# Kernel tuning notes

Hardware: AMD Instinct MI355X
Metric: run time of the kernel (lower is better)

The kernel has to match this reference:

```python
import jax, jax.numpy as jnp
import numpy as np

N_HEADS = 8
EPS = 1e-8


def _build_gp_map():
    # Cl(4,1) geometric-product structure constants. Blade index = 5-bit mask,
    # e1..e5 = bits 0..4; metric (+,+,+,+,-): e5 (bit 4) squares to -1.
    def pc(n):
        return bin(n).count("1")
    g = np.zeros((32, 32, 32), np.float32)
    for a in range(32):
        for b in range(32):
            swaps = 0
            aa = a >> 1
            while aa:
                swaps += pc(aa & b)
                aa >>= 1
            sign = -1.0 if (swaps & 1) else 1.0
            if (a & b) & 0b10000:  # shared e5 factor contributes -1
                sign = -sign
            g[a, b, a ^ b] = sign
    return g

GP_MAP = jnp.asarray(_build_gp_map())          # (32,32,32)
BIVEC_IDX = jnp.array([3, 5, 6, 9, 10, 12, 17, 18, 20, 24])  # grade-2 blades
SCALAR_VECTOR_IDX = np.array([0, 1, 2, 4, 8, 16])            # grade-0 + grade-1


def normalize_cl41(x):
    return x / jnp.sqrt(jnp.sum(x * x, axis=-1, keepdims=True) + EPS)


def geometric_linear(w, x):
    # w: (O,I,32), x: (...,I,32) -> (...,O,32)
    wg = jnp.einsum('oij,jlk->oilk', w, GP_MAP)     # fold gp_map into weight
    out = jnp.einsum('oilk,...il->...ok', wg, x)
    return normalize_cl41(out)


def _init_weight(key, out_f, in_f):
    # Grade-aware Xavier: only scalar + vector lanes are nonzero.
    std = 1.0 / np.sqrt(in_f * 32)
    vals = jax.random.normal(key, (out_f, in_f, len(SCALAR_VECTOR_IDX)), jnp.float32) * std
    w = jnp.zeros((out_f, in_f, 32), jnp.float32)
    return w.at[:, :, SCALAR_VECTOR_IDX].set(vals)


def setup_inputs() -> dict:
    key = jax.random.key(0)
    kx, kq, kk, kv, ko = jax.random.split(key, 5)
    B, S, D = 2, 384, 128
    x = jax.random.normal(kx, (B, S, D, 32), jnp.float32)
    return {
        'x': x,
        'wq': _init_weight(kq, D, D),
        'wk': _init_weight(kk, D, D),
        'wv': _init_weight(kv, D, D),
        'wo': _init_weight(ko, D, D),
        'attn_lambda': jnp.float32(0.1),
    }


def reference(x, wq, wk, wv, wo, attn_lambda):
    B, S, D, _ = x.shape
    H = N_HEADS
    hd = D // H
    def split_heads(t):  # (B,S,D,32) -> (B,H,S,hd,32)
        return t.reshape(B, S, H, hd, 32).transpose(0, 2, 1, 3, 4)
    q = split_heads(geometric_linear(wq, x))
    k = split_heads(geometric_linear(wk, x))
    v = split_heads(geometric_linear(wv, x))

    # Geometric product Q*K contracted over head_dim, then over gp_map lanes.
    qg = jnp.einsum('bhsdi,ijk->bhsdjk', q, GP_MAP)      # (B,H,S,hd,32,32)
    raw_mv = jnp.einsum('bhsdjk,bhxdj->bhsxk', qg, k)    # (B,H,S,S,32)
    raw_mv = normalize_cl41(raw_mv)

    scalar_part = raw_mv[..., 0]
    biv = raw_mv[..., BIVEC_IDX]
    bivector_norm = jnp.sqrt(jnp.sum(biv * biv, axis=-1) + EPS)
    score = (scalar_part + attn_lambda * bivector_norm) / np.sqrt(hd).astype(np.float32)
    attn_probs = jax.nn.softmax(score, axis=-1)          # (B,H,S,S)

    out = jnp.einsum('bhsx,bhxdl->bhsdl', attn_probs, v)  # (B,H,S,hd,32)
    out = out.transpose(0, 2, 1, 3, 4).reshape(B, S, D, 32)
    return geometric_linear(wo, out)
```

## Files before the change

kernel.cpp:

```cpp
#include <hip/hip_runtime.h>
#include <math.h>

#define BB    2
#define SS    384
#define DD    128
#define NH    8
#define HDIM  16
#define NBH   16
#define BS    768

typedef unsigned int   u32;
typedef unsigned short u16;
typedef __attribute__((ext_vector_type(8))) short short8;
typedef __attribute__((ext_vector_type(4))) float f32x4;

struct SignTab { float v[32][32]; };
constexpr int popcnt32c(int x){ int c=0; for(int i=0;i<32;i++) c += (x>>i)&1; return c; }
constexpr int signgp_int(int a, int b){
  int swaps=0; int aa=a>>1;
  while(aa){ swaps += popcnt32c(aa & b); aa >>= 1; }
  int s = (swaps & 1) ? -1 : 1;
  if ((a & b) & 16) s = -s;
  return s;
}
constexpr SignTab make_signs(){
  SignTab t{};
  for(int a=0;a<32;a++) for(int b=0;b<32;b++)
    t.v[a][b] = (float)signgp_int(a,b);
  return t;
}
constexpr SignTab GPS = make_signs();

struct MaskTab { u32 v[4][8][4][4]; };
constexpr MaskTab mkmask(){
  MaskTab t{};
  for(int w=0;w<4;w++) for(int u=0;u<8;u++) for(int q=0;q<4;q++) for(int r=0;r<4;r++){
    u32 m = 0;
    for(int h=0;h<2;h++){
      int j = 2*r + h;
      int i = (q<<3) | j;
      int c = (w<<3) | u;
      if (signgp_int(i, i^c) < 0) m |= (h ? 0x80000000u : 0x8000u);
    }
    t.v[w][u][q][r] = m;
  }
  return t;
}
constexpr MaskTab MT = mkmask();

__device__ __forceinline__ u16 f2bf(float f){
  u32 x = __float_as_uint(f);
  return (u16)((x + 0x7FFFu + ((x>>16)&1u)) >> 16);
}
__device__ __forceinline__ float bf2f(u16 h){
  return __uint_as_float(((u32)h) << 16);
}

__global__ __launch_bounds__(256) void repack_wb(const float* __restrict__ wq,
                                                 const float* __restrict__ wk,
                                                 const float* __restrict__ wv,
                                                 const float* __restrict__ wo,
                                                 u16* __restrict__ wpk2){
  int idx = blockIdx.x*256 + threadIdx.x;
  int p = blockIdx.y;
  const float* w = (p==0)?wq:(p==1)?wk:(p==2)?wv:wo;
  int o   = idx / 768;
  int rem = idx - o*768;
  int jp  = rem >> 7;
  int i   = rem & 127;
  const int SV[6] = {0,1,2,4,8,16};
  wpk2[p*98304 + idx] = f2bf(w[(o*128 + i)*32 + SV[jp]]);
}

#define XLS 33
__global__ __launch_bounds__(256) void gather_k(const void* __restrict__ src,
                                                int src_bf16,
                                                u16* __restrict__ xg){
  __shared__ float xl[2*128*XLS];
  int t = threadIdx.x;
  int bs0 = blockIdx.x*2;
  int bsl = t >> 7, i = t & 127;

  float row[32];
  if (src_bf16){
    const uint4* s4 = (const uint4*)((const u16*)src + (((size_t)(bs0+bsl)*128 + i)*32));
    #pragma unroll
    for(int r=0;r<4;r++){
      uint4 v = s4[r];
      u32 ww[4] = {v.x,v.y,v.z,v.w};
      #pragma unroll
      for(int h=0;h<4;h++){
        row[r*8 + 2*h    ] = __uint_as_float(ww[h] << 16);
        row[r*8 + 2*h + 1] = __uint_as_float(ww[h] & 0xFFFF0000u);
      }
    }
  } else {
    const float4* s4 = (const float4*)((const float*)src + (((size_t)(bs0+bsl)*128 + i)*32));
    #pragma unroll
    for(int r=0;r<8;r++){
      float4 v = s4[r];
      row[r*4+0]=v.x; row[r*4+1]=v.y; row[r*4+2]=v.z; row[r*4+3]=v.w;
    }
  }
  float* xrow = xl + bsl*128*XLS + i*XLS;
  #pragma unroll
  for(int l=0;l<32;l++) xrow[l] = row[l];
  __syncthreads();

  const int SV[6] = {0,1,2,4,8,16};
  u32* xg32 = (u32*)xg;
  #pragma unroll 4
  for(int r=0;r<96;r++){
    int wr = t + r*256;
    int k   = wr / 768;
    int rem = wr - k*768;
    int bl  = rem / 384;
    int r2  = rem - bl*384;
    int jp  = r2 >> 6;
    int ip  = r2 & 63;
    int i2  = ip*2;
    int b   = SV[jp] ^ k;
    float sg = GPS.v[SV[jp]][b];
    const float* base = xl + bl*128*XLS;
    float f0 = base[ i2   *XLS + b] * sg;
    float f1 = base[(i2+1)*XLS + b] * sg;
    u32 pk = (u32)f2bf(f0) | ((u32)f2bf(f1) << 16);
    xg32[((size_t)k*768 + bs0 + bl)*384 + jp*64 + ip] = pk;
  }
}

#define LSTR 40
__global__ __launch_bounds__(256) void gemm_proj(const u16* __restrict__ xg,
                                                 const u16* __restrict__ wpkA,
                                                 u16* __restrict__ tmpA){
  __shared__ __align__(16) u16 As[128*LSTR];
  __shared__ __align__(16) u16 Bs[128*LSTR];
  int t = threadIdx.x;
  int Mt = blockIdx.x, k = blockIdx.y, p = blockIdx.z;
  const u16* wpk = wpkA + (size_t)p*98304;
  u16* tmp = tmpA + (size_t)p*32*768*128;

  int w = t >> 6, lane = t & 63;
  int q = lane >> 4, n16 = lane & 15;
  int wm = w >> 1, wn = w & 1;

  f32x4 acc[4][4];
  #pragma unroll
  for(int a=0;a<4;a++)
    #pragma unroll
    for(int b=0;b<4;b++) acc[a][b] = (f32x4){0.f,0.f,0.f,0.f};

  int r0 = t>>2, c0 = (t&3)*8;
  int r1 = (t+256)>>2, c1 = ((t+256)&3)*8;
  const u16* Aab = xg + ((size_t)k*768 + Mt*128)*768;

  uint4 pa0, pa1, pb0, pb1;
  {
    pa0 = *(const uint4*)(Aab + (size_t)r0*768 + c0);
    pa1 = *(const uint4*)(Aab + (size_t)r1*768 + c1);
    pb0 = *(const uint4*)(wpk + (size_t)r0*768 + c0);
    pb1 = *(const uint4*)(wpk + (size_t)r1*768 + c1);
  }

  for(int kt=0; kt<24; kt++){
    __syncthreads();
    *(uint4*)(As + r0*LSTR + c0) = pa0;
    *(uint4*)(As + r1*LSTR + c1) = pa1;
    *(uint4*)(Bs + r0*LSTR + c0) = pb0;
    *(uint4*)(Bs + r1*LSTR + c1) = pb1;
    __syncthreads();
    if (kt < 23){
      int kn = (kt+1)*32;
      pa0 = *(const uint4*)(Aab + (size_t)r0*768 + kn + c0);
      pa1 = *(const uint4*)(Aab + (size_t)r1*768 + kn + c1);
      pb0 = *(const uint4*)(wpk + (size_t)r0*768 + kn + c0);
      pb1 = *(const uint4*)(wpk + (size_t)r1*768 + kn + c1);
    }
    short8 a[4], b[4];
    #pragma unroll
    for(int mi=0;mi<4;mi++)
      a[mi] = *(const short8*)(As + (wm*64 + mi*16 + n16)*LSTR + q*8);
    #pragma unroll
    for(int ni=0;ni<4;ni++)
      b[ni] = *(const short8*)(Bs + (wn*64 + ni*16 + n16)*LSTR + q*8);
    #pragma unroll
    for(int mi=0;mi<4;mi++)
      #pragma unroll
      for(int ni=0;ni<4;ni++)
        acc[mi][ni] = __builtin_amdgcn_mfma_f32_16x16x32_bf16(a[mi], b[ni], acc[mi][ni], 0,0,0);
  }

  #pragma unroll
  for(int mi=0;mi<4;mi++){
    #pragma unroll
    for(int r=0;r<4;r++){
      int m = Mt*128 + wm*64 + mi*16 + q*4 + r;
      #pragma unroll
      for(int ni=0;ni<4;ni++){
        int n = wn*64 + ni*16 + n16;
        tmp[((size_t)k*768 + m)*128 + n] = f2bf(acc[mi][ni][r]);
      }
    }
  }
}

__global__ __launch_bounds__(256) void norm3(const u16* __restrict__ tmpA,
                                             u16* __restrict__ qhb,
                                             u16* __restrict__ khb,
                                             u16* __restrict__ vbb){
  int z = blockIdx.y;
  const u16* tmp = tmpA + (size_t)z*32*768*128;
  u16* dst = (z==0)?qhb:(z==1)?khb:vbb;
  int t = threadIdx.x;
  int bsl = t >> 7, o = t & 127;
  int bs = blockIdx.x*2 + bsl;

  float a[32];
  float ssum = 1e-8f;
  #pragma unroll
  for(int k=0;k<32;k++){
    a[k] = bf2f(tmp[((size_t)k*768 + bs)*128 + o]);
    ssum = fmaf(a[k], a[k], ssum);
  }
  float inv = 1.0f / sqrtf(ssum);

  int b = bs / SS, s = bs - b*SS;
  int h = o >> 4, d = o & 15;
  uint4* og4 = (uint4*)(dst + (((size_t)(b*NH + h)*SS + s)*512 + d*32));
  #pragma unroll
  for(int l=0;l<4;l++){
    uint4 v;
    v.x = (u32)f2bf(a[8*l+0]*inv) | ((u32)f2bf(a[8*l+1]*inv)<<16);
    v.y = (u32)f2bf(a[8*l+2]*inv) | ((u32)f2bf(a[8*l+3]*inv)<<16);
    v.z = (u32)f2bf(a[8*l+4]*inv) | ((u32)f2bf(a[8*l+5]*inv)<<16);
    v.w = (u32)f2bf(a[8*l+6]*inv) | ((u32)f2bf(a[8*l+7]*inv)<<16);
    og4[l] = v;
  }
}

__global__ __launch_bounds__(256) void norm_out(const u16* __restrict__ tmp,
                                                float* __restrict__ dst){
  int t = threadIdx.x;
  int bsl = t >> 7, o = t & 127;
  int bs = blockIdx.x*2 + bsl;

  float a[32];
  float ssum = 1e-8f;
  #pragma unroll
  for(int k=0;k<32;k++){
    a[k] = bf2f(tmp[((size_t)k*768 + bs)*128 + o]);
    ssum = fmaf(a[k], a[k], ssum);
  }
  float inv = 1.0f / sqrtf(ssum);
  float4* og = (float4*)(dst + ((size_t)bs*128 + o)*32);
  #pragma unroll
  for(int l4=0;l4<8;l4++){
    float4 v;
    v.x = a[4*l4+0]*inv; v.y = a[4*l4+1]*inv;
    v.z = a[4*l4+2]*inv; v.w = a[4*l4+3]*inv;
    og[l4] = v;
  }
}

#define TVS 528
__global__ __launch_bounds__(256) void transpose_v(const u16* __restrict__ vb,
                                                   u16* __restrict__ vt){
  __shared__ __align__(16) u16 vl[32*TVS];
  int t = threadIdx.x;
  int xt = blockIdx.x, bh = blockIdx.y;
  const u16* src = vb + ((size_t)bh*SS + xt*32)*512;
  #pragma unroll
  for(int j=0;j<8;j++){
    int f = t + j*256; int row = f>>6, c = (f&63)*8;
    *(uint4*)(vl + row*TVS + c) = *(const uint4*)(src + (size_t)row*512 + c);
  }
  __syncthreads();
  u16* dst = vt + (size_t)bh*512*SS + xt*32;
  #pragma unroll
  for(int j=0;j<8;j++){
    int f = t + j*256; int dl = f>>2, c4 = (f&3)*8;
    u16 tmp[8];
    #pragma unroll
    for(int e=0;e<8;e++) tmp[e] = vl[(c4+e)*TVS + dl];
    *(uint4*)(dst + (size_t)dl*SS + c4) = *(uint4*)tmp;
  }
}

#define QSTR 264
__global__ __launch_bounds__(256,2) void scores_mfma(const u16* __restrict__ qh,
                                                     const u16* __restrict__ kh,
                                                     float* __restrict__ sc,
                                                     const float* __restrict__ lam){
  __shared__ __align__(16) u16 smem[(64+16)*QSTR];
  u16* qs = smem;
  u16* ks = smem + 64*QSTR;
  int t = threadIdx.x;
  int xt = blockIdx.x, st = blockIdx.y, bh = blockIdx.z;
  int w = t >> 6, lane = t & 63, q = lane >> 4, mn = lane & 15;

  u32 FM[8][4];
  #pragma unroll
  for(int u=0;u<8;u++)
    #pragma unroll
    for(int r=0;r<4;r++) FM[u][r] = MT.v[w][u][q][r];

  f32x4 acc[4][8];
  #pragma unroll
  for(int mi=0;mi<4;mi++)
    #pragma unroll
    for(int u=0;u<8;u++) acc[mi][u] = (f32x4){0.f,0.f,0.f,0.f};

  for(int h=0; h<2; h++){
    __syncthreads();
    const u16* qbase = qh + ((size_t)bh*SS + st*64)*512 + h*256;
    const u16* kbase = kh + ((size_t)bh*SS + xt*16)*512 + h*256;
    #pragma unroll
    for(int j=0;j<8;j++){
      int f = t + j*256;
      int row = f>>5, c = (f&31)*8;
      *(uint4*)(qs + row*QSTR + c) = *(const uint4*)(qbase + (size_t)row*512 + c);
    }
    #pragma unroll
    for(int j=0;j<2;j++){
      int f = t + j*256;
      int row = f>>5, c = (f&31)*8;
      *(uint4*)(ks + row*QSTR + c) = *(const uint4*)(kbase + (size_t)row*512 + c);
    }
    __syncthreads();

    for(int ktl=0; ktl<8; ktl++){
      short8 a[4];
      #pragma unroll
      for(int mi=0;mi<4;mi++)
        a[mi] = *(const short8*)(qs + (mi*16+mn)*QSTR + ktl*32 + q*8);
      uint4 khd = *(const uint4*)(ks + mn*QSTR + ktl*32 + ((q^w)<<3));
      u32 kk[4] = {khd.x, khd.y, khd.z, khd.w};
      #pragma unroll
      for(int u=0;u<8;u++){
        union { u32 w32[4]; short8 s; } bf;
        #pragma unroll
        for(int r=0;r<4;r++){
          u32 v = kk[r ^ (u>>1)];
          if (u & 1) v = (v>>16)|(v<<16);
          bf.w32[r] = v ^ FM[u][r];
        }
        #pragma unroll
        for(int mi=0;mi<4;mi++)
          acc[mi][u] = __builtin_amdgcn_mfma_f32_16x16x32_bf16(a[mi], bf.s, acc[mi][u], 0, 0, 0);
      }
    }
  }
  __syncthreads();

  float* pss = (float*)smem;
  float* pbb = pss + 4*64*17;
  float* ps0 = pbb + 4*64*17;

  #pragma unroll
  for(int mi=0;mi<4;mi++){
    #pragma unroll
    for(int rr=0;rr<4;rr++){
      float ssv = 0.f, bbv = 0.f;
      #pragma unroll
      for(int u=0;u<8;u++){
        int c = w*8 + u;
        bool isb = (c==3)||(c==5)||(c==6)||(c==9)||(c==10)||(c==12)||
                   (c==17)||(c==18)||(c==20)||(c==24);
        float v = acc[mi][u][rr];
        ssv = fmaf(v, v, ssv);
        if (isb) bbv = fmaf(v, v, bbv);
      }
      int s = mi*16 + q*4 + rr;
      pss[(w*64 + s)*17 + mn] = ssv;
      pbb[(w*64 + s)*17 + mn] = bbv;
      if (w == 0) ps0[s*17 + mn] = acc[mi][0][rr];
    }
  }
  __syncthreads();

  int x = t & 15, s0 = t >> 4;
  float lm = lam[0];
  #pragma unroll
  for(int ssi=0; ssi<4; ssi++){
    int s = s0 + ssi*16;
    float ss = 1e-8f, bb = 0.f;
    #pragma unroll
    for(int ww=0; ww<4; ww++){
      ss += pss[(ww*64+s)*17+x];
      bb += pbb[(ww*64+s)*17+x];
    }
    float inv = 1.0f / sqrtf(ss);
    float s0v = ps0[s*17+x];
    float score = (s0v*inv + lm*sqrtf(bb*inv*inv + 1e-8f)) * 0.25f;
    sc[((size_t)bh*SS + st*64 + s)*SS + xt*16 + x] = score;
  }
}

#define PBS 392
#define VSS 40
__global__ __launch_bounds__(256,2) void pv_mfma(const float* __restrict__ sc,
                                                 const u16* __restrict__ vt,
                                                 u16* __restrict__ om){
  __shared__ __align__(16) u16 pb[16*PBS];
  __shared__ __align__(16) u16 vsm[512*VSS];
  int t = threadIdx.x;
  int st = blockIdx.x, bh = blockIdx.y;
  int w = t >> 6, lane = t & 63, q = lane >> 4, mn = lane & 15;

  {
    int row = t >> 4, g = t & 15;
    const float* srow = sc + ((size_t)bh*SS + st*16 + row)*SS;
    float v[24];
    float mx = -1e30f;
    #pragma unroll
    for(int k2=0;k2<24;k2++){ v[k2] = srow[g + k2*16]; mx = fmaxf(mx, v[k2]); }
    #pragma unroll
    for(int off=8; off; off>>=1) mx = fmaxf(mx, __shfl_xor(mx, off));
    float sum = 0.f;
    #pragma unroll
    for(int k2=0;k2<24;k2++){ v[k2] = __expf(v[k2]-mx); sum += v[k2]; }
    #pragma unroll
    for(int off=8; off; off>>=1) sum += __shfl_xor(sum, off);
    float inv = 1.f/sum;
    #pragma unroll
    for(int k2=0;k2<24;k2++) pb[row*PBS + g + k2*16] = f2bf(v[k2]*inv);
  }

  f32x4 acc[8];
  #pragma unroll
  for(int mt=0;mt<8;mt++) acc[mt] = (f32x4){0.f,0.f,0.f,0.f};

  const u16* vtb = vt + (size_t)bh*512*SS;
  for(int kt=0; kt<12; kt++){
    __syncthreads();
    #pragma unroll
    for(int j=0;j<8;j++){
      int f = t + j*256;
      int dl = f>>2, c4 = (f&3)*8;
      *(uint4*)(vsm + dl*VSS + c4) = *(const uint4*)(vtb + (size_t)dl*SS + kt*32 + c4);
    }
    __syncthreads();
    short8 b = *(const short8*)(pb + mn*PBS + kt*32 + q*8);
    #pragma unroll
    for(int mt=0;mt<8;mt++){
      short8 a = *(const short8*)(vsm + ((w*8+mt)*16 + mn)*VSS + q*8);
      acc[mt] = __builtin_amdgcn_mfma_f32_16x16x32_bf16(a, b, acc[mt], 0, 0, 0);
    }
  }
  __syncthreads();

  float* ot = (float*)vsm;
  #pragma unroll
  for(int mt=0;mt<8;mt++)
    #pragma unroll
    for(int rr=0;rr<4;rr++)
      ot[((w*8+mt)*16 + q*4 + rr)*17 + mn] = acc[mt][rr];
  __syncthreads();

  int b = bh >> 3, h = bh & 7;
  u32* om32 = (u32*)om;
  #pragma unroll
  for(int j=0;j<16;j++){
    int f = t + j*256;
    int s = f >> 8, dlp = f & 255, dl = dlp*2;
    float f0 = ot[dl*17 + s], f1 = ot[(dl+1)*17 + s];
    u32 pk = (u32)f2bf(f0) | ((u32)f2bf(f1) << 16);
    int sg = st*16 + s;
    om32[(size_t)(b*SS + sg)*2048 + h*256 + dlp] = pk;
  }
}

extern "C" void kernel_launch(void* const* d_in, const int* in_sizes, int n_in,
                              void* d_out, int out_size, void* d_ws, size_t ws_size,
                              hipStream_t stream) {
  const float* x   = (const float*)d_in[0];
  const float* wq  = (const float*)d_in[1];
  const float* wk  = (const float*)d_in[2];
  const float* wv  = (const float*)d_in[3];
  const float* wo  = (const float*)d_in[4];
  const float* lam = (const float*)d_in[5];
  float* out = (float*)d_out;

  char* ws = (char*)d_ws;
  size_t off = 0;
  u16*   wpk2 = (u16*)(ws + off); off += (size_t)4*98304*2;
  u16*   xg   = (u16*)(ws + off); off += (size_t)32*768*768*2;
  float* sc   = (float*)xg;
  u16*   tmp3 = (u16*)(ws + off); off += (size_t)3*32*768*128*2;
  u16*   vt   = tmp3;
  u16*   qhb  = (u16*)(ws + off); off += (size_t)NBH*SS*512*2;
  u16*   khb  = (u16*)(ws + off); off += (size_t)NBH*SS*512*2;
  u16*   vb   = (u16*)(ws + off); off += (size_t)NBH*SS*512*2;
  u16*   om   = (u16*)(ws + off); off += (size_t)BS*128*32*2;

  repack_wb<<<dim3(384,4),256,0,stream>>>(wq, wk, wv, wo, wpk2);
  gather_k<<<384,256,0,stream>>>(x, 0, xg);
  gemm_proj<<<dim3(6,32,3),256,0,stream>>>(xg, wpk2, tmp3);
  norm3<<<dim3(384,3),256,0,stream>>>(tmp3, qhb, khb, vb);
  transpose_v<<<dim3(12,16),256,0,stream>>>(vb, vt);

  scores_mfma<<<dim3(24,6,16),256,0,stream>>>(qhb, khb, sc, lam);
  pv_mfma<<<dim3(24,16),256,0,stream>>>(sc, vt, om);

  gather_k<<<384,256,0,stream>>>(om, 1, xg);
  gemm_proj<<<dim3(6,32,1),256,0,stream>>>(xg, wpk2 + (size_t)3*98304, tmp3);
  norm_out<<<384,256,0,stream>>>(tmp3, out);
}
```

Measured before the change: 264.1 us.

## Swizzle scores LDS tiles, load full K once, prefetch V tiles in registers

In the scores kernel, the padded LDS layout is replaced with an XOR-swizzled layout, and the full 512-wide K tile is loaded once instead of per half. The halfword-swapped K words are precomputed once per k-step. In the attention-V kernel, the next V tile is prefetched into registers while the current tile is consumed, overlapping global loads with MFMA work. This adds register pressure, which may reduce occupancy under the 256,2 launch bounds.

```diff
diff --git a/kernel.cpp b/kernel.cpp
--- a/kernel.cpp
+++ b/kernel.cpp
@@ -286,17 +286,17 @@
   }
 }
 
-#define QSTR 264
 __global__ __launch_bounds__(256,2) void scores_mfma(const u16* __restrict__ qh,
                                                      const u16* __restrict__ kh,
                                                      float* __restrict__ sc,
                                                      const float* __restrict__ lam){
-  __shared__ __align__(16) u16 smem[(64+16)*QSTR];
+  __shared__ __align__(16) u16 smem[64*256 + 16*512];
   u16* qs = smem;
-  u16* ks = smem + 64*QSTR;
+  u16* ks = smem + 64*256;
   int t = threadIdx.x;
   int xt = blockIdx.x, st = blockIdx.y, bh = blockIdx.z;
   int w = t >> 6, lane = t & 63, q = lane >> 4, mn = lane & 15;
+  float lm = lam[0];
 
   u32 FM[8][4];
   #pragma unroll
@@ -304,44 +304,53 @@
     #pragma unroll
     for(int r=0;r<4;r++) FM[u][r] = MT.v[w][u][q][r];
 
+  const u16* kbase = kh + ((size_t)bh*SS + xt*16)*512;
+  #pragma unroll
+  for(int j=0;j<4;j++){
+    int f = t + j*256;
+    int row = f >> 6, c = f & 63;
+    int p = c ^ (row & 7);
+    *(uint4*)(ks + row*512 + p*8) = *(const uint4*)(kbase + (size_t)row*512 + c*8);
+  }
+
   f32x4 acc[4][8];
   #pragma unroll
   for(int mi=0;mi<4;mi++)
     #pragma unroll
     for(int u=0;u<8;u++) acc[mi][u] = (f32x4){0.f,0.f,0.f,0.f};
+
+  const u16* qbase = qh + ((size_t)bh*SS + st*64)*512;
 
   for(int h=0; h<2; h++){
     __syncthreads();
-    const u16* qbase = qh + ((size_t)bh*SS + st*64)*512 + h*256;
-    const u16* kbase = kh + ((size_t)bh*SS + xt*16)*512 + h*256;
     #pragma unroll
     for(int j=0;j<8;j++){
       int f = t + j*256;
-      int row = f>>5, c = (f&31)*8;
-      *(uint4*)(qs + row*QSTR + c) = *(const uint4*)(qbase + (size_t)row*512 + c);
-    }
-    #pragma unroll
-    for(int j=0;j<2;j++){
-      int f = t + j*256;
-      int row = f>>5, c = (f&31)*8;
-      *(uint4*)(ks + row*QSTR + c) = *(const uint4*)(kbase + (size_t)row*512 + c);
+      int row = f >> 5, c = f & 31;
+      int p = c ^ (row & 7);
+      *(uint4*)(qs + row*256 + p*8) = *(const uint4*)(qbase + (size_t)row*512 + h*256 + c*8);
     }
     __syncthreads();
 
     for(int ktl=0; ktl<8; ktl++){
       short8 a[4];
       #pragma unroll
-      for(int mi=0;mi<4;mi++)
-        a[mi] = *(const short8*)(qs + (mi*16+mn)*QSTR + ktl*32 + q*8);
-      uint4 khd = *(const uint4*)(ks + mn*QSTR + ktl*32 + ((q^w)<<3));
-      u32 kk[4] = {khd.x, khd.y, khd.z, khd.w};
+      for(int mi=0;mi<4;mi++){
+        int pc = (ktl*4 + q) ^ (mn & 7);
+        a[mi] = *(const short8*)(qs + (mi*16+mn)*256 + pc*8);
+      }
+      int kc = (h*32 + ktl*4 + (q^w)) ^ (mn & 7);
+      uint4 khd = *(const uint4*)(ks + mn*512 + kc*8);
+      u32 kk[4]  = {khd.x, khd.y, khd.z, khd.w};
+      u32 kks[4];
+      #pragma unroll
+      for(int r=0;r<4;r++) kks[r] = (kk[r]>>16)|(kk[r]<<16);
       #pragma unroll
       for(int u=0;u<8;u++){
         union { u32 w32[4]; short8 s; } bf;
         #pragma unroll
         for(int r=0;r<4;r++){
-          u32 v = kk[r ^ (u>>1)];
-          if (u & 1) v = (v>>16)|(v<<16);
+          u32 v = (u & 1) ? kks[r ^ (u>>1)] : kk[r ^ (u>>1)];
           bf.w32[r] = v ^ FM[u][r];
         }
         #pragma unroll
@@ -379,7 +388,6 @@
   __syncthreads();
 
   int x = t & 15, s0 = t >> 4;
-  float lm = lam[0];
   #pragma unroll
   for(int ssi=0; ssi<4; ssi++){
     int s = s0 + ssi*16;
@@ -431,15 +439,24 @@
   for(int mt=0;mt<8;mt++) acc[mt] = (f32x4){0.f,0.f,0.f,0.f};
 
   const u16* vtb = vt + (size_t)bh*512*SS;
+  int dl0 = t >> 2, c40 = (t & 3)*8;
+
+  uint4 pf[8];
+  #pragma unroll
+  for(int j=0;j<8;j++)
+    pf[j] = *(const uint4*)(vtb + (size_t)(dl0 + j*64)*SS + c40);
+
   for(int kt=0; kt<12; kt++){
     __syncthreads();
     #pragma unroll
-    for(int j=0;j<8;j++){
-      int f = t + j*256;
-      int dl = f>>2, c4 = (f&3)*8;
-      *(uint4*)(vsm + dl*VSS + c4) = *(const uint4*)(vtb + (size_t)dl*SS + kt*32 + c4);
-    }
+    for(int j=0;j<8;j++)
+      *(uint4*)(vsm + (dl0 + j*64)*VSS + c40) = pf[j];
     __syncthreads();
+    if (kt < 11){
+      #pragma unroll
+      for(int j=0;j<8;j++)
+        pf[j] = *(const uint4*)(vtb + (size_t)(dl0 + j*64)*SS + (kt+1)*32 + c40);
+    }
     short8 b = *(const short8*)(pb + mn*PBS + kt*32 + q*8);
     #pragma unroll
     for(int mt=0;mt<8;mt++){
```

New measurement: 309.5 us. 1.17x slower.
